# Optimization experiments

Measured on AMD Instinct MI355X. Metric: run time of the kernel, lower is better.

Reference implementation:

```python
import jax, jax.numpy as jnp
import numpy as np

B, T, C, H = 2, 4096, 768, 12
D = C // H  # head_dim = 64


def setup_inputs() -> dict:
    key = jax.random.key(0)
    k1, k2, k3 = jax.random.split(key, 3)
    x = jax.random.normal(k1, (B, T, C), dtype=jnp.float32)
    w_qkv = jax.random.normal(k2, (C, 3 * C), dtype=jnp.float32) * (1.0 / np.sqrt(C))
    w_out = jax.random.normal(k3, (C, C), dtype=jnp.float32) * (1.0 / np.sqrt(C))
    return {"x": x, "w_qkv": w_qkv, "w_out": w_out}


def reference(x, w_qkv, w_out):
    b, t, c = x.shape
    qkv = x @ w_qkv                              # (B,T,3C)
    q, k, v = jnp.split(qkv, 3, axis=-1)
    # (B,T,C) -> (B,H,T,D)
    q = q.reshape(b, t, H, D).transpose(0, 2, 1, 3)
    k = k.reshape(b, t, H, D).transpose(0, 2, 1, 3)
    v = v.reshape(b, t, H, D).transpose(0, 2, 1, 3)
    att = jnp.einsum('bhqd,bhkd->bhqk', q, k) / jnp.sqrt(jnp.float32(D))
    causal = jnp.tril(jnp.ones((t, t), dtype=bool))  # True where allowed
    att = jnp.where(causal, att, -jnp.inf)
    att = jax.nn.softmax(att, axis=-1)
    y = jnp.einsum('bhqk,bhkd->bhqd', att, v)        # (B,H,T,D)
    y = y.transpose(0, 2, 1, 3).reshape(b, t, c)
    return y @ w_out
```

## Files before the change

### kernel.cpp

```cpp
#include <hip/hip_runtime.h>
#include <stdint.h>
#include <stddef.h>

#define NB 2
#define NT 4096
#define NC 768
#define NH 12
#define ND 64

typedef unsigned short u16;
typedef __attribute__((ext_vector_type(2))) float f32x2;
typedef __attribute__((ext_vector_type(4))) float f32x4;
typedef __attribute__((ext_vector_type(16))) float f32x16;
typedef __attribute__((ext_vector_type(8))) unsigned short u16x8;
typedef __attribute__((ext_vector_type(4))) unsigned short u16x4;
typedef __attribute__((ext_vector_type(8))) __bf16 bf16x8;
typedef __attribute__((ext_vector_type(4))) unsigned int u32x4;

typedef __attribute__((address_space(1))) const unsigned int gu32;
typedef __attribute__((address_space(3))) unsigned int lu32;

__device__ __forceinline__ u16 f2bf(float f) {
  uint32_t u = __builtin_bit_cast(uint32_t, f);
  u += 0x7FFFu + ((u >> 16) & 1u);
  return (u16)(u >> 16);
}
__device__ __forceinline__ bf16x8 asbf(u16x8 v) { return __builtin_bit_cast(bf16x8, v); }

__device__ __forceinline__ uint32_t pkbf(float a, float b) {
  uint32_t ua = __builtin_bit_cast(uint32_t, a) + 0x8000u;
  uint32_t ub = __builtin_bit_cast(uint32_t, b) + 0x8000u;
  return __builtin_amdgcn_perm(ub, ua, 0x07060302u);
}
__device__ __forceinline__ uint32_t pktr(float a, float b) {
  return __builtin_amdgcn_perm(__builtin_bit_cast(uint32_t, b),
                               __builtin_bit_cast(uint32_t, a), 0x07060302u);
}

#define GLDS(gsrc, ldst) __builtin_amdgcn_global_load_lds( \
    (gu32*)(gsrc), (lu32*)(ldst), 16, 0, 0)

#define PRE_CAST_BLKS 6144
#define PRE_TA_BX 72
#define PRE_TA_BLKS (72 * 24)
#define PRE_TB_BX 24
#define PRE_TB_BLKS (24 * 24)
__global__ __launch_bounds__(256)
void k_pre(const float* __restrict__ x, u16* __restrict__ xb,
           const float* __restrict__ w_qkv, u16* __restrict__ wqT,
           const float* __restrict__ w_out, u16* __restrict__ woT) {
  __shared__ float tile[32][33];
  const int bid = blockIdx.x;
  const int tid = threadIdx.x;
  if (bid < PRE_CAST_BLKS) {
    int i = bid * 256 + tid;
    f32x4 v = ((const f32x4*)x)[i];
    u16x4 o;
    o[0] = f2bf(v[0]); o[1] = f2bf(v[1]); o[2] = f2bf(v[2]); o[3] = f2bf(v[3]);
    ((u16x4*)xb)[i] = o;
    return;
  }
  const float* in;
  u16* out;
  int R, Cn, bx, by;
  if (bid < PRE_CAST_BLKS + PRE_TA_BLKS) {
    int q = bid - PRE_CAST_BLKS;
    bx = q % PRE_TA_BX; by = q / PRE_TA_BX;
    in = w_qkv; out = wqT; R = NC; Cn = 3 * NC;
  } else {
    int q = bid - PRE_CAST_BLKS - PRE_TA_BLKS;
    bx = q % PRE_TB_BX; by = q / PRE_TB_BX;
    in = w_out; out = woT; R = NC; Cn = NC;
  }
  int c0 = bx * 32, r0 = by * 32;
  int tx = tid & 31, ty = tid >> 5;
  for (int i = ty; i < 32; i += 8)
    tile[i][tx] = in[(size_t)(r0 + i) * Cn + c0 + tx];
  __syncthreads();
  for (int i = ty; i < 32; i += 8)
    out[(size_t)(c0 + i) * R + r0 + tx] = f2bf(tile[tx][i]);
}

template <int EPI>
__global__ __launch_bounds__(256, 3)
void k_gemm_bt(const u16* __restrict__ A, const u16* __restrict__ Bt,
               int M, int N, int K,
               u16* __restrict__ o0, u16* __restrict__ o1, u16* __restrict__ o2,
               float* __restrict__ of) {
  __shared__ u16 SMEM[2 * 128 * 64];
  u16* As = SMEM;
  u16* Bs = SMEM + 8192;
  const int tid = threadIdx.x;
  const int wave = tid >> 6, lane = tid & 63, quad = lane >> 4, lc = lane & 15;
  const int wm = (wave & 1) * 64, wn = (wave >> 1) * 64;
  const int bm = blockIdx.y * 128, bn = blockIdx.x * 128;

  const int lr = lane >> 3;
  const int gsw = ((lane & 7) ^ lr) * 8;
  const int rB = wave * 8 + lr;
  const u16* gA = A + (size_t)(bm + rB) * K + gsw;
  const u16* gB = Bt + (size_t)(bn + rB) * K + gsw;
  u16* lA0 = &As[wave * 8 * 64];
  u16* lB0 = &Bs[wave * 8 * 64];

  f32x4 zv = {0.f, 0.f, 0.f, 0.f};
  f32x4 acc[4][4];
#pragma unroll
  for (int i = 0; i < 4; ++i)
#pragma unroll
    for (int j = 0; j < 4; ++j) acc[i][j] = zv;

  for (int k0 = 0; k0 < K; k0 += 64) {
    __syncthreads();
#pragma unroll
    for (int c = 0; c < 4; ++c) {
      GLDS(gA + (size_t)c * 32 * K + k0, lA0 + c * 2048);
      GLDS(gB + (size_t)c * 32 * K + k0, lB0 + c * 2048);
    }
    asm volatile("s_waitcnt vmcnt(0)" ::: "memory");
    __syncthreads();

#pragma unroll
    for (int ks = 0; ks < 2; ++ks) {
      const int ao = (((ks << 2) + quad) ^ (lc & 7)) * 8;
      bf16x8 af[4], bfv[4];
#pragma unroll
      for (int mi = 0; mi < 4; ++mi)
        af[mi] = asbf(*(const u16x8*)&As[(wm + mi * 16 + lc) * 64 + ao]);
#pragma unroll
      for (int ni = 0; ni < 4; ++ni)
        bfv[ni] = asbf(*(const u16x8*)&Bs[(wn + ni * 16 + lc) * 64 + ao]);
#pragma unroll
      for (int mi = 0; mi < 4; ++mi)
#pragma unroll
        for (int ni = 0; ni < 4; ++ni)
          acc[mi][ni] = __builtin_amdgcn_mfma_f32_16x16x32_bf16(af[mi], bfv[ni],
                                                                acc[mi][ni], 0, 0, 0);
    }
  }

  const int sect = (EPI == 1) ? (bn / NC) : 0;
  if (EPI == 1 && sect == 2) {
    const int b = bm >> 12;
    const int tb = bm & (NT - 1);
    const int hb = (bn - 2 * NC) >> 6;
#pragma unroll 1
    for (int r2_ = 0; r2_ < 2; ++r2_) {
      __syncthreads();
      if ((wave >> 1) == r2_) {
#pragma unroll
        for (int mi = 0; mi < 4; ++mi)
#pragma unroll
          for (int ni = 0; ni < 4; ++ni) {
            const int nl = ni * 16 + lc;
#pragma unroll
            for (int r = 0; r < 4; ++r) {
              const int m = wm + mi * 16 + quad * 4 + r;
              SMEM[nl * 128 + (m ^ ((nl & 7) << 3))] = f2bf(acc[mi][ni][r]);
            }
          }
      }
      __syncthreads();
#pragma unroll
      for (int pass = 0; pass < 4; ++pass) {
        const int row = (tid >> 4) + 16 * pass;
        const int chunk = tid & 15;
        u16x8 w = *(const u16x8*)&SMEM[row * 128 + ((chunk ^ (row & 7)) * 8)];
        const int nl = 64 * r2_ + row;
        *(u16x8*)&o2[((size_t)(b * NH + hb + (nl >> 6)) * ND + (nl & 63)) * NT
                     + tb + chunk * 8] = w;
      }
    }
    return;
  }

  const int mrow0 = bm + wm + quad * 4;
#pragma unroll
  for (int mi = 0; mi < 4; ++mi) {
    const int mbase = mrow0 + mi * 16;
#pragma unroll
    for (int ni = 0; ni < 4; ++ni) {
      const int n = bn + wn + ni * 16 + lc;
      if (EPI == 0) {
#pragma unroll
        for (int r = 0; r < 4; ++r)
          of[(size_t)(mbase + r) * N + n] = acc[mi][ni][r];
      } else {
        const int wn2 = n - sect * NC;
        const int h = wn2 >> 6, d = wn2 & 63;
        const int b = mbase >> 12;
        const int t = mbase & (NT - 1);
        const float sc = (sect == 0) ? 0.18033688011112042f : 1.0f;
        u16* dst = (sect == 0) ? o0 : o1;
#pragma unroll
        for (int r = 0; r < 4; ++r)
          dst[((size_t)(b * NH + h) * NT + (t + r)) * ND + d] =
              f2bf(acc[mi][ni][r] * sc);
      }
    }
  }
}

__device__ __forceinline__ void softpack16(const f32x16& s, int qrel, bool msk,
                                           int l5, f32x2& sl2, bf16x8* pf) {
  float e[16];
#pragma unroll
  for (int r = 0; r < 16; ++r) {
    float v = s[r];
    if (msk) {
      int tl = (r & 3) + 8 * (r >> 2) + 4 * l5;
      v = (tl > qrel) ? -1e30f : v;
    }
    e[r] = __builtin_amdgcn_exp2f(v);
  }
  uint32_t wv[8];
#pragma unroll
  for (int i = 0; i < 8; ++i) {
    wv[i] = pktr(e[2 * i], e[2 * i + 1]);
    f32x2 inc = {__builtin_bit_cast(float, wv[i] & 0xFFFF0000u),
                 __builtin_bit_cast(float, wv[i] << 16)};
    sl2 += inc;
  }
#pragma unroll
  for (int g = 0; g < 2; ++g) {
    auto r0 = __builtin_amdgcn_permlane32_swap(wv[g * 4 + 0], wv[g * 4 + 2], false, false);
    auto r1 = __builtin_amdgcn_permlane32_swap(wv[g * 4 + 1], wv[g * 4 + 3], false, false);
    u32x4 f = {r0[0], r1[0], r0[1], r1[1]};
    pf[g] = __builtin_bit_cast(bf16x8, f);
  }
}

__global__ __launch_bounds__(256, 3)
void k_attn(const u16* __restrict__ Q, const u16* __restrict__ K,
            const u16* __restrict__ Vt, u16* __restrict__ Y) {
  __shared__ u16 SM[2][64 * 64];
  __shared__ float PL[2][64];
  const int tid = threadIdx.x;
  const int lane = tid & 63, wave = tid >> 6;
  const int l5 = lane >> 5, l31 = lane & 31;
  const int qh = wave & 1, th = wave >> 1;
  const int bh = blockIdx.x % (NB * NH);
  const int qi = 63 - blockIdx.x / (NB * NH);
  const int b = bh / NH, h = bh - b * NH;
  const u16* __restrict__ Qb = Q + (size_t)bh * NT * ND;
  const u16* __restrict__ Kb = K + (size_t)bh * NT * ND;
  const u16* __restrict__ Vb = Vt + (size_t)bh * (size_t)ND * NT;

  const int qg = qi * 64 + qh * 32 + l31;

  bf16x8 bq[4];
#pragma unroll
  for (int ks = 0; ks < 4; ++ks)
    bq[ks] = asbf(*(const u16x8*)(Qb + (size_t)qg * ND + ks * 16 + l5 * 8));

  f32x16 Zv;
#pragma unroll
  for (int i = 0; i < 16; ++i) Zv[i] = 0.f;
  f32x16 o0 = Zv, o1 = Zv;
  f32x2 sl2 = {0.f, 0.f};

  const int srow = tid >> 3, sg = tid & 7;
  const int soff = srow * 64 + ((sg ^ (srow & 7)) * 8);
  const u16* __restrict__ pK = Kb + (size_t)srow * ND + sg * 8;
  const u16* __restrict__ pV = Vb + (size_t)srow * NT + sg * 8;

  int qfro[4];
#pragma unroll
  for (int ks = 0; ks < 4; ++ks)
    qfro[ks] = (th * 32 + l31) * 64 + (((ks * 2 + l5) ^ (l31 & 7)) * 8);
  int vfro[2];
#pragma unroll
  for (int kp = 0; kp < 2; ++kp)
    vfro[kp] = l31 * 64 + ((((2 * th + kp) * 2 + l5) ^ (l31 & 7)) * 8);

  u16x8 st[4];
  st[0] = *(const u16x8*)(pK);
  st[1] = *(const u16x8*)(pK + (size_t)32 * ND);
  st[2] = *(const u16x8*)(pV);
  st[3] = *(const u16x8*)(pV + (size_t)32 * NT);

#pragma unroll 1
  for (int tau = 0; tau <= qi; ++tau) {
    __syncthreads();
    *(u16x8*)&SM[0][soff] = st[0];
    *(u16x8*)&SM[0][2048 + soff] = st[1];
    *(u16x8*)&SM[1][soff] = st[2];
    *(u16x8*)&SM[1][2048 + soff] = st[3];
    __syncthreads();

    const bool dg = (tau == qi);
    const bool act = !(dg && th > qh);
    bf16x8 p[2];
    if (act) {
      bf16x8 kf0 = asbf(*(const u16x8*)&SM[0][qfro[0]]);
      __builtin_amdgcn_s_setprio(1);
      f32x16 s = __builtin_amdgcn_mfma_f32_32x32x16_bf16(kf0, bq[0], Zv, 0, 0, 0);
#pragma unroll
      for (int ks = 1; ks < 4; ++ks) {
        bf16x8 kf = asbf(*(const u16x8*)&SM[0][qfro[ks]]);
        s = __builtin_amdgcn_mfma_f32_32x32x16_bf16(kf, bq[ks], s, 0, 0, 0);
      }
      __builtin_amdgcn_s_setprio(0);
      softpack16(s, l31, dg && (th == qh), l5, sl2, p);
    }

    if (tau < qi) {
      const int tn = (tau + 1) * 64;
      st[0] = *(const u16x8*)(pK + (size_t)tn * ND);
      st[1] = *(const u16x8*)(pK + (size_t)(tn + 32) * ND);
      st[2] = *(const u16x8*)(pV + tn);
      st[3] = *(const u16x8*)(pV + (size_t)32 * NT + tn);
    }

    if (act) {
      __builtin_amdgcn_s_setprio(1);
#pragma unroll
      for (int kp = 0; kp < 2; ++kp) {
        bf16x8 v0 = asbf(*(const u16x8*)&SM[1][vfro[kp]]);
        bf16x8 v1 = asbf(*(const u16x8*)&SM[1][2048 + vfro[kp]]);
        o0 = __builtin_amdgcn_mfma_f32_32x32x16_bf16(v0, p[kp], o0, 0, 0, 0);
        o1 = __builtin_amdgcn_mfma_f32_32x32x16_bf16(v1, p[kp], o1, 0, 0, 0);
      }
      __builtin_amdgcn_s_setprio(0);
    }
  }

  const float slv = sl2[0] + sl2[1];
  float l = slv + __shfl_xor(slv, 32);
  __syncthreads();
  float* PK = (float*)&SM[0][0];
  if (th == 0) {
#pragma unroll
    for (int r = 0; r < 16; ++r) PK[(qh * 32 + r) * 64 + lane] = o0[r];
#pragma unroll
    for (int r = 0; r < 16; ++r) PK[(qh * 32 + 16 + r) * 64 + lane] = o1[r];
    PL[qh][lane] = l;
  }
  __syncthreads();
  if (th == 1) {
#pragma unroll
    for (int r = 0; r < 16; ++r) o0[r] += PK[(qh * 32 + r) * 64 + lane];
#pragma unroll
    for (int r = 0; r < 16; ++r) o1[r] += PK[(qh * 32 + 16 + r) * 64 + lane];
    l += PL[qh][lane];
    const float inv = 1.f / l;
    u16* yrow = Y + (size_t)(b * NT + qg) * NC + h * 64;
#pragma unroll
    for (int dh = 0; dh < 2; ++dh) {
      const f32x16& o = dh ? o1 : o0;
#pragma unroll
      for (int rq = 0; rq < 4; ++rq) {
        const int d = dh * 32 + 8 * rq + 4 * l5;
        uint2 w;
        w.x = pkbf(o[rq * 4 + 0] * inv, o[rq * 4 + 1] * inv);
        w.y = pkbf(o[rq * 4 + 2] * inv, o[rq * 4 + 3] * inv);
        *(uint2*)&yrow[d] = w;
      }
    }
  }
}

extern "C" void kernel_launch(void* const* d_in, const int* in_sizes, int n_in,
                              void* d_out, int out_size, void* d_ws, size_t ws_size,
                              hipStream_t stream) {
  (void)in_sizes; (void)n_in; (void)out_size; (void)ws_size;
  const float* x = (const float*)d_in[0];
  const float* w_qkv = (const float*)d_in[1];
  const float* w_out = (const float*)d_in[2];
  float* out = (float*)d_out;

  u16* ws = (u16*)d_ws;
  const size_t XE = (size_t)NB * NT * NC;
  u16* xb  = ws;
  u16* wqT = xb + XE;
  u16* woT = wqT + (size_t)3 * NC * NC;
  u16* Qb  = woT + (size_t)NC * NC;
  u16* Kb  = Qb + XE;
  u16* Vtb = Kb + XE;
  u16* yb  = Vtb + XE;

  k_pre<<<dim3(PRE_CAST_BLKS + PRE_TA_BLKS + PRE_TB_BLKS), 256, 0, stream>>>(
      x, xb, w_qkv, wqT, w_out, woT);
  k_gemm_bt<1><<<dim3(3 * NC / 128, NB * NT / 128), 256, 0, stream>>>(
      xb, wqT, NB * NT, 3 * NC, NC, Qb, Kb, Vtb, nullptr);
  k_attn<<<dim3((NB * NH) * 64), 256, 0, stream>>>(Qb, Kb, Vtb, yb);
  k_gemm_bt<0><<<dim3(NC / 128, NB * NT / 128), 256, 0, stream>>>(
      yb, woT, NB * NT, NC, NC, nullptr, nullptr, nullptr, out);
}
```

Before: 221.2 us.

## Double-buffer attention K/V via direct global-to-LDS loads and remap GEMM blocks per XCD

The attention kernel replaces its register-staged K/V tile loads with direct global-to-LDS loads (GLDS) into a double-buffered shared-memory region. The next tile is prefetched while the current one is computed, using vmcnt waits and raw barriers in place of two __syncthreads per iteration. Separately, the GEMM launches become 1D grids with a workgroup-id remap that spreads consecutive tiles across the 8 XCDs, aiming for better L2 locality. This doubles the attention LDS footprint, which may lower occupancy, and it relies on the GLDS macro and waitcnt counts being correct.

After: 222.0 us. Within noise of the previous version (+0.4%).

```diff
diff --git a/kernel.cpp b/kernel.cpp
--- a/kernel.cpp
+++ b/kernel.cpp
@@ -81,7 +81,7 @@
     out[(size_t)(c0 + i) * R + r0 + tx] = f2bf(tile[tx][i]);
 }
 
-template <int EPI>
+template <int EPI, int NBX>
 __global__ __launch_bounds__(256, 3)
 void k_gemm_bt(const u16* __restrict__ A, const u16* __restrict__ Bt,
                int M, int N, int K,
@@ -93,7 +93,10 @@
   const int tid = threadIdx.x;
   const int wave = tid >> 6, lane = tid & 63, quad = lane >> 4, lc = lane & 15;
   const int wm = (wave & 1) * 64, wn = (wave >> 1) * 64;
-  const int bm = blockIdx.y * 128, bn = blockIdx.x * 128;
+  const int wg = blockIdx.x;
+  const int nid = (wg & 7) * ((int)gridDim.x >> 3) + (wg >> 3);
+  const int bx = nid % NBX, by = nid / NBX;
+  const int bm = by * 128, bn = bx * 128;
 
   const int lr = lane >> 3;
   const int gsw = ((lane & 7) ^ lr) * 8;
@@ -233,7 +236,7 @@
 __global__ __launch_bounds__(256, 3)
 void k_attn(const u16* __restrict__ Q, const u16* __restrict__ K,
             const u16* __restrict__ Vt, u16* __restrict__ Y) {
-  __shared__ u16 SM[2][64 * 64];
+  __shared__ u16 RAW[2 * 8192];
   __shared__ float PL[2][64];
   const int tid = threadIdx.x;
   const int lane = tid & 63, wave = tid >> 6;
@@ -259,10 +262,15 @@
   f32x16 o0 = Zv, o1 = Zv;
   f32x2 sl2 = {0.f, 0.f};
 
-  const int srow = tid >> 3, sg = tid & 7;
-  const int soff = srow * 64 + ((sg ^ (srow & 7)) * 8);
-  const u16* __restrict__ pK = Kb + (size_t)srow * ND + sg * 8;
-  const u16* __restrict__ pV = Vb + (size_t)srow * NT + sg * 8;
+  const int lr = lane >> 3;
+  const int gsw = ((lane & 7) ^ lr) * 8;
+  const int r0w = wave * 16;
+  const u16* gk0 = Kb + (size_t)(r0w + lr) * ND + gsw;
+  const u16* gk1 = gk0 + (size_t)8 * ND;
+  const u16* gv0 = Vb + (size_t)(r0w + lr) * NT + gsw;
+  const u16* gv1 = gv0 + (size_t)8 * NT;
+  u16* lk = &RAW[r0w * 64];
+  u16* lv = &RAW[4096 + r0w * 64];
 
   int qfro[4];
 #pragma unroll
@@ -271,64 +279,62 @@
   int vfro[2];
 #pragma unroll
   for (int kp = 0; kp < 2; ++kp)
-    vfro[kp] = l31 * 64 + ((((2 * th + kp) * 2 + l5) ^ (l31 & 7)) * 8);
-
-  u16x8 st[4];
-  st[0] = *(const u16x8*)(pK);
-  st[1] = *(const u16x8*)(pK + (size_t)32 * ND);
-  st[2] = *(const u16x8*)(pV);
-  st[3] = *(const u16x8*)(pV + (size_t)32 * NT);
+    vfro[kp] = 4096 + l31 * 64 + ((((2 * th + kp) * 2 + l5) ^ (l31 & 7)) * 8);
+
+  GLDS(gk0, lk);
+  GLDS(gk1, lk + 512);
+  GLDS(gv0, lv);
+  GLDS(gv1, lv + 512);
 
 #pragma unroll 1
   for (int tau = 0; tau <= qi; ++tau) {
-    __syncthreads();
-    *(u16x8*)&SM[0][soff] = st[0];
-    *(u16x8*)&SM[0][2048 + soff] = st[1];
-    *(u16x8*)&SM[1][soff] = st[2];
-    *(u16x8*)&SM[1][2048 + soff] = st[3];
-    __syncthreads();
+    const int p = tau & 1;
+    if (tau < qi) {
+      const int tn = (tau + 1) * 64;
+      const int bo = (p ^ 1) * 8192;
+      GLDS(gk0 + (size_t)tn * ND, lk + bo);
+      GLDS(gk1 + (size_t)tn * ND, lk + bo + 512);
+      GLDS(gv0 + tn, lv + bo);
+      GLDS(gv1 + tn, lv + bo + 512);
+      asm volatile("s_waitcnt vmcnt(4)" ::: "memory");
+    } else {
+      asm volatile("s_waitcnt vmcnt(0)" ::: "memory");
+    }
+    __builtin_amdgcn_s_barrier();
 
     const bool dg = (tau == qi);
     const bool act = !(dg && th > qh);
-    bf16x8 p[2];
     if (act) {
-      bf16x8 kf0 = asbf(*(const u16x8*)&SM[0][qfro[0]]);
+      const u16* bufp = &RAW[p * 8192];
+      bf16x8 kf0 = asbf(*(const u16x8*)&bufp[qfro[0]]);
       __builtin_amdgcn_s_setprio(1);
       f32x16 s = __builtin_amdgcn_mfma_f32_32x32x16_bf16(kf0, bq[0], Zv, 0, 0, 0);
 #pragma unroll
       for (int ks = 1; ks < 4; ++ks) {
-        bf16x8 kf = asbf(*(const u16x8*)&SM[0][qfro[ks]]);
+        bf16x8 kf = asbf(*(const u16x8*)&bufp[qfro[ks]]);
         s = __builtin_amdgcn_mfma_f32_32x32x16_bf16(kf, bq[ks], s, 0, 0, 0);
       }
       __builtin_amdgcn_s_setprio(0);
-      softpack16(s, l31, dg && (th == qh), l5, sl2, p);
-    }
-
-    if (tau < qi) {
-      const int tn = (tau + 1) * 64;
-      st[0] = *(const u16x8*)(pK + (size_t)tn * ND);
-      st[1] = *(const u16x8*)(pK + (size_t)(tn + 32) * ND);
-      st[2] = *(const u16x8*)(pV + tn);
-      st[3] = *(const u16x8*)(pV + (size_t)32 * NT + tn);
-    }
-
-    if (act) {
+      bf16x8 p2[2];
+      softpack16(s, l31, dg && (th == qh), l5, sl2, p2);
+
       __builtin_amdgcn_s_setprio(1);
 #pragma unroll
       for (int kp = 0; kp < 2; ++kp) {
-        bf16x8 v0 = asbf(*(const u16x8*)&SM[1][vfro[kp]]);
-        bf16x8 v1 = asbf(*(const u16x8*)&SM[1][2048 + vfro[kp]]);
-        o0 = __builtin_amdgcn_mfma_f32_32x32x16_bf16(v0, p[kp], o0, 0, 0, 0);
-        o1 = __builtin_amdgcn_mfma_f32_32x32x16_bf16(v1, p[kp], o1, 0, 0, 0);
+        bf16x8 v0 = asbf(*(const u16x8*)&bufp[vfro[kp]]);
+        bf16x8 v1 = asbf(*(const u16x8*)&bufp[vfro[kp] + 2048]);
+        o0 = __builtin_amdgcn_mfma_f32_32x32x16_bf16(v0, p2[kp], o0, 0, 0, 0);
+        o1 = __builtin_amdgcn_mfma_f32_32x32x16_bf16(v1, p2[kp], o1, 0, 0, 0);
       }
       __builtin_amdgcn_s_setprio(0);
     }
+    __builtin_amdgcn_s_barrier();
   }
 
   const float slv = sl2[0] + sl2[1];
   float l = slv + __shfl_xor(slv, 32);
   __syncthreads();
-  float* PK = (float*)&SM[0][0];
+  float* PK = (float*)&RAW[0];
   if (th == 0) {
 #pragma unroll
     for (int r = 0; r < 16; ++r) PK[(qh * 32 + r) * 64 + lane] = o0[r];
@@ -381,9 +387,9 @@
 
   k_pre<<<dim3(PRE_CAST_BLKS + PRE_TA_BLKS + PRE_TB_BLKS), 256, 0, stream>>>(
       x, xb, w_qkv, wqT, w_out, woT);
-  k_gemm_bt<1><<<dim3(3 * NC / 128, NB * NT / 128), 256, 0, stream>>>(
+  k_gemm_bt<1, 18><<<dim3(18 * 64), 256, 0, stream>>>(
       xb, wqT, NB * NT, 3 * NC, NC, Qb, Kb, Vtb, nullptr);
   k_attn<<<dim3((NB * NH) * 64), 256, 0, stream>>>(Qb, Kb, Vtb, yb);
-  k_gemm_bt<0><<<dim3(NC / 128, NB * NT / 128), 256, 0, stream>>>(
+  k_gemm_bt<0, 6><<<dim3(6 * 64), 256, 0, stream>>>(
       yb, woT, NB * NT, NC, NC, nullptr, nullptr, nullptr, out);
 }
```
